# Optimization experiments

Hardware: AMD Instinct MI355X
Metric: run time of the kernel (lower is better)

## Reference

```python
import jax, jax.numpy as jnp
import numpy as np

B, T, P, H, LAT = 64, 256, 128, 512, 128


def _run_lstm(x, Wih, Whh, b, h0, c0):
    """Single unidirectional LSTM layer, PyTorch gate order (i,f,g,o).
    x: (B,T,in) -> outputs (B,T,H), final h (B,H)."""
    xW = jnp.einsum('bti,gi->btg', x, Wih) + b  # precompute input projection (B,T,4H)

    def step(carry, xw_t):
        h, c = carry
        g = xw_t + h @ Whh.T
        i, f, gg, o = jnp.split(g, 4, axis=-1)
        c = jax.nn.sigmoid(f) * c + jax.nn.sigmoid(i) * jnp.tanh(gg)
        h = jax.nn.sigmoid(o) * jnp.tanh(c)
        return (h, c), h

    (hT, cT), hs = jax.lax.scan(step, (h0, c0), jnp.swapaxes(xW, 0, 1))
    return jnp.swapaxes(hs, 0, 1), hT


def setup_inputs() -> dict:
    key = jax.random.key(0)
    ks = iter(jax.random.split(key, 40))
    rn = lambda shape, s=0.05: jax.random.normal(next(ks), shape, jnp.float32) * s
    inp = {
        'x': (jax.random.uniform(next(ks), (B, T, P)) < 0.1).astype(jnp.float32),
        'e0f_Wih': rn((4 * H, P)), 'e0f_Whh': rn((4 * H, H)), 'e0f_b': jnp.zeros((4 * H,), jnp.float32),
        'e0b_Wih': rn((4 * H, P)), 'e0b_Whh': rn((4 * H, H)), 'e0b_b': jnp.zeros((4 * H,), jnp.float32),
        'e1f_Wih': rn((4 * H, 2 * H)), 'e1f_Whh': rn((4 * H, H)), 'e1f_b': jnp.zeros((4 * H,), jnp.float32),
        'e1b_Wih': rn((4 * H, 2 * H)), 'e1b_Whh': rn((4 * H, H)), 'e1b_b': jnp.zeros((4 * H,), jnp.float32),
        'enc_fc_W': rn((LAT, 2 * H)), 'enc_fc_b': jnp.zeros((LAT,), jnp.float32),
        'dec_fc_W': rn((H, LAT)), 'dec_fc_b': jnp.zeros((H,), jnp.float32),
        'start_token': rn((1, 1, P), 0.1),
        'd0_Wih': rn((4 * H, P)), 'd0_Whh': rn((4 * H, H)), 'd0_b': jnp.zeros((4 * H,), jnp.float32),
        'd1_Wih': rn((4 * H, H)), 'd1_Whh': rn((4 * H, H)), 'd1_b': jnp.zeros((4 * H,), jnp.float32),
        'out_W': rn((P, H)), 'out_b': jnp.zeros((P,), jnp.float32),
        'teacher_forcing_ratio': 1,
    }
    return inp


def reference(x, e0f_Wih, e0f_Whh, e0f_b, e0b_Wih, e0b_Whh, e0b_b,
              e1f_Wih, e1f_Whh, e1f_b, e1b_Wih, e1b_Whh, e1b_b,
              enc_fc_W, enc_fc_b, dec_fc_W, dec_fc_b, start_token,
              d0_Wih, d0_Whh, d0_b, d1_Wih, d1_Whh, d1_b, out_W, out_b,
              teacher_forcing_ratio):
    b = x.shape[0]
    z0 = jnp.zeros((b, H), x.dtype)
    # ---- encoder: 2-layer bidirectional LSTM ----
    f0, _ = _run_lstm(x, e0f_Wih, e0f_Whh, e0f_b, z0, z0)
    r0, _ = _run_lstm(x[:, ::-1], e0b_Wih, e0b_Whh, e0b_b, z0, z0)
    l0 = jnp.concatenate([f0, r0[:, ::-1]], axis=-1)  # (B,T,2H)
    _, h_fwd = _run_lstm(l0, e1f_Wih, e1f_Whh, e1f_b, z0, z0)
    _, h_bwd = _run_lstm(l0[:, ::-1], e1b_Wih, e1b_Whh, e1b_b, z0, z0)
    z = jnp.concatenate([h_fwd, h_bwd], axis=-1) @ enc_fc_W.T + enc_fc_b  # (B,LAT)
    # ---- decoder: teacher-forced 2-layer LSTM ----
    h0d = z @ dec_fc_W.T + dec_fc_b  # (B,H), repeated for every layer
    xs = jnp.concatenate([jnp.broadcast_to(start_token, (b, 1, P)), x[:, :-1]], axis=1)
    o0, _ = _run_lstm(xs, d0_Wih, d0_Whh, d0_b, h0d, z0)
    o1, _ = _run_lstm(o0, d1_Wih, d1_Whh, d1_b, h0d, z0)
    x_hat = jax.nn.sigmoid(o1 @ out_W.T + out_b)  # (B,T,P)
    return x_hat, z
```

## Files before the change

kernel.cpp:

```cpp
#include <hip/hip_runtime.h>
#include <stdint.h>


typedef unsigned short u16;
typedef unsigned int u32;
typedef float f32x4 __attribute__((ext_vector_type(4)));
typedef __bf16 bf16x8 __attribute__((ext_vector_type(8)));
typedef unsigned int u32x4 __attribute__((ext_vector_type(4)));

#define AT_LD(p) __hip_atomic_load((p), __ATOMIC_RELAXED, __HIP_MEMORY_SCOPE_AGENT)
#define AT_ST(p, v) __hip_atomic_store((p), (v), __ATOMIC_RELAXED, __HIP_MEMORY_SCOPE_AGENT)

__device__ __forceinline__ u16 f2bf(float f) {
  u32 u = __builtin_bit_cast(u32, f);
  u += 0x7FFFu + ((u >> 16) & 1u);
  return (u16)(u >> 16);
}
__device__ __forceinline__ float bf2f(u16 h) {
  return __builtin_bit_cast(float, (u32)h << 16);
}
__device__ __forceinline__ bf16x8 ld8(const u16* p) {
  u32x4 v = *(const u32x4*)p;
  return __builtin_bit_cast(bf16x8, v);
}
__device__ __forceinline__ float sigf(float x) { return 1.f / (1.f + __expf(-x)); }
__device__ __forceinline__ float tanhx(float x) {
  x = fminf(fmaxf(x, -15.f), 15.f);
  float e = __expf(2.f * x);
  return (e - 1.f) / (e + 1.f);
}

__global__ void k_prep_x(const float* __restrict__ x, const float* __restrict__ st,
                         u16* __restrict__ Ax, u16* __restrict__ Axs, int n) {
  int i = blockIdx.x * 256 + threadIdx.x;
  if (i >= n) return;
  Ax[i] = f2bf(x[i]);
  int col = i & 127;
  int t = (i >> 7) & 255;
  float v = (t == 0) ? st[col] : x[i - 128];
  Axs[i] = f2bf(v);
}

struct CvtJobs {
  const float* src[13];
  u16* dst[13];
  int off[14];
};
__global__ void k_cvt_all(CvtJobs j, int total) {
  int i = blockIdx.x * 256 + threadIdx.x;
  if (i >= total) return;
  int a = 0;
#pragma unroll
  for (int k = 1; k < 13; ++k) a += (i >= j.off[k]) ? 1 : 0;
  int local = i - j.off[a];
  j.dst[a][local] = f2bf(j.src[a][local]);
}

__global__ __launch_bounds__(256) void k_gemm_bt(
    const u16* __restrict__ A, const u16* __restrict__ B, const float* __restrict__ bias,
    u16* __restrict__ Cb, float* __restrict__ Cf, int M, int N, int K, int sig) {
  __shared__ __align__(16) u16 As[128 * 64];
  __shared__ __align__(16) u16 Bs[128 * 64];
  const int m0 = blockIdx.x * 128, n0 = blockIdx.y * 128;
  const int tid = threadIdx.x, lane = tid & 63, wave = tid >> 6;
  const int wm = wave >> 1, wn = wave & 1;

  f32x4 acc[4][4];
#pragma unroll
  for (int i = 0; i < 4; ++i)
#pragma unroll
    for (int j = 0; j < 4; ++j) acc[i][j] = (f32x4){0.f, 0.f, 0.f, 0.f};

  const int nkt = K >> 6;
  for (int kt = 0; kt < nkt; ++kt) {
#pragma unroll
    for (int i = 0; i < 4; ++i) {
      int ch = tid + (i << 8);
      int row = ch >> 3, k8 = ch & 7;
      int dst = row * 128 + ((k8 * 16) ^ ((row & 7) << 4));
      u32x4 va = *(const u32x4*)(A + (size_t)(m0 + row) * K + kt * 64 + k8 * 8);
      *(u32x4*)((char*)As + dst) = va;
      u32x4 vb = *(const u32x4*)(B + (size_t)(n0 + row) * K + kt * 64 + k8 * 8);
      *(u32x4*)((char*)Bs + dst) = vb;
    }
    __syncthreads();
#pragma unroll
    for (int kk = 0; kk < 2; ++kk) {
      int kb = kk * 64 + ((lane >> 4) << 4);
      bf16x8 afr[4], bfr[4];
#pragma unroll
      for (int i = 0; i < 4; ++i) {
        int ra = wm * 64 + i * 16 + (lane & 15);
        afr[i] = ld8((const u16*)((const char*)As + ra * 128 + (kb ^ ((ra & 7) << 4))));
        int rb = wn * 64 + i * 16 + (lane & 15);
        bfr[i] = ld8((const u16*)((const char*)Bs + rb * 128 + (kb ^ ((rb & 7) << 4))));
      }
#pragma unroll
      for (int i = 0; i < 4; ++i)
#pragma unroll
        for (int j = 0; j < 4; ++j)
          acc[i][j] = __builtin_amdgcn_mfma_f32_16x16x32_bf16(afr[i], bfr[j], acc[i][j], 0, 0, 0);
    }
    __syncthreads();
  }
#pragma unroll
  for (int i = 0; i < 4; ++i) {
#pragma unroll
    for (int j = 0; j < 4; ++j) {
      int col = n0 + wn * 64 + j * 16 + (lane & 15);
      float bv = bias ? bias[col] : 0.f;
#pragma unroll
      for (int r = 0; r < 4; ++r) {
        int row = m0 + wm * 64 + i * 16 + ((lane >> 4) << 2) + r;
        float v = acc[i][j][r] + bv;
        if (sig) Cf[(size_t)row * N + col] = 1.f / (1.f + __expf(-v));
        else     Cb[(size_t)row * N + col] = f2bf(v);
      }
    }
  }
}

struct Rec2 {
  const u16* xW[8];
  const u16* Whh[8];
  const u16* Wih[8];
  const float* bias[8];
  const float* h0[8];
  u16* seq[8];
  float* hfin[8];
  u16* hxc[8];
  int prod[8];
  int seqstride[8]; int coloff[8]; int rev[8]; int hfinstride[8];
  int grp[8]; int fused[8]; int fullp[8];
  u32* tags;
};

__global__ __launch_bounds__(256, 1) void k_rec2(Rec2 p) {
  const int chain = blockIdx.x & 7;
  const int c = blockIdx.x >> 3;
  const int tid = threadIdx.x, lane = tid & 63, wave = tid >> 6;
  const int arow = lane & 15, kg = lane >> 4;

  const u16* __restrict__ xW = p.xW[chain];
  const u16* __restrict__ Whh = p.Whh[chain];
  const u16* __restrict__ Wih = p.Wih[chain];
  const float* __restrict__ bias = p.bias[chain];
  const float* __restrict__ h0 = p.h0[chain];
  u16* seq = p.seq[chain];
  float* hfin = p.hfin[chain];
  u32* hx = (u32*)p.hxc[chain];
  const u32* hxp = (const u32*)p.hxc[p.prod[chain]];
  const int grp = p.grp[chain], rev = p.rev[chain];
  const int fused = p.fused[chain], fullp = p.fullp[chain];
  const int sstride = p.seqstride[chain], coloff = p.coloff[chain];
  const int hstride = p.hfinstride[chain];
  u32* myt = p.tags + chain * 64;
  const u32* pt = p.tags + p.prod[chain] * 64;

  __shared__ __align__(16) u16 Wlds[64][64][8];
  __shared__ __align__(16) u16 Xlds[64][64][8];
  __shared__ __align__(16) u16 hbufA[8192];
  __shared__ float gbuf[4][16][16];
  __shared__ float cbuf[256];
  __shared__ float bbuf[64];

  for (int e = tid; e < 4096; e += 256) {
    int n = e >> 6, k8 = e & 63;
    int grow = ((n >> 4) << 9) + (c << 4) + (n & 15);
    *(u32x4*)(&Wlds[k8][n][0]) = *(const u32x4*)(Whh + (size_t)grow * 512 + k8 * 8);
    if (fused)
      *(u32x4*)(&Xlds[k8][n][0]) = *(const u32x4*)(Wih + (size_t)grow * 512 + k8 * 8);
  }
  if (tid < 64) bbuf[tid] = fused ? bias[((tid >> 4) << 9) + (c << 4) + (tid & 15)] : 0.f;
  cbuf[tid] = 0.f;
  if (tid < 128) {
    int row = tid >> 3, q = tid & 7;
    float a = 0.f, b2 = 0.f;
    if (h0) {
      a = h0[(size_t)(grp * 16 + row) * 512 + (c << 4) + 2 * q];
      b2 = h0[(size_t)(grp * 16 + row) * 512 + (c << 4) + 2 * q + 1];
    }
    u32 pk = (u32)f2bf(a) | ((u32)f2bf(b2) << 16);
    AT_ST(hx + (size_t)c * 128 + (row << 3) + q, pk);
  }
  asm volatile("s_waitcnt vmcnt(0)" ::: "memory");
  __syncthreads();
  if (tid == 0) AT_ST(myt + c, 1u);

  for (int t = 0; t < 256; ++t) {
    const int t_eff = rev ? 255 - t : t;
    const int slot = fullp ? t : (t & 3);
    const int slotn = fullp ? (t + 1) : ((t + 1) & 3);

    float xwv[4] = {0.f, 0.f, 0.f, 0.f};
    if (!fused) {
#pragma unroll
      for (int r4 = 0; r4 < 4; ++r4) {
        int row = (kg << 2) + r4;
        xwv[r4] = bf2f(xW[(((size_t)((grp * 16 + row) * 256 + t_eff)) << 11) +
                          (wave << 9) + (c << 4) + arow]);
      }
    }
    if (wave == 0) {
      u32 thr_own = (u32)(t + 1), thr_prod = (u32)(t + 2);
      while (true) {
        int ok = 1;
        if (lane < 32) {
          if (lane != c) ok = (AT_LD(myt + lane) >= thr_own);
        } else if (fused) {
          ok = (AT_LD(pt + (lane - 32)) >= thr_prod);
        }
        if (__all(ok)) break;
        __builtin_amdgcn_s_sleep(1);
      }
    }
    __syncthreads();
    __builtin_amdgcn_sched_barrier(0);

#pragma unroll
    for (int i = 0; i < 4; ++i) {
      int cid = tid + (i << 8);
      int row = cid >> 6, ch8 = cid & 63;
      const u32* src = hx + ((size_t)slot * 32 + (ch8 >> 1)) * 128 +
                       (row << 3) + ((ch8 & 1) << 2);
      u32x4 v;
      v.x = AT_LD(src + 0); v.y = AT_LD(src + 1);
      v.z = AT_LD(src + 2); v.w = AT_LD(src + 3);
      *(u32x4*)((char*)hbufA + row * 1024 + ((ch8 << 4) ^ ((row & 7) << 4))) = v;
    }
    bf16x8 xf[16];
    if (fused) {
#pragma unroll
      for (int kt = 0; kt < 16; ++kt) {
        const u32* hp = hxp + ((size_t)(t + 1) * 32 + 2 * kt + (kg >> 1)) * 128 +
                        (arow << 3) + ((kg & 1) << 2);
        u32x4 v;
        v.x = AT_LD(hp + 0); v.y = AT_LD(hp + 1);
        v.z = AT_LD(hp + 2); v.w = AT_LD(hp + 3);
        xf[kt] = __builtin_bit_cast(bf16x8, v);
      }
    }
    __syncthreads();

    bf16x8 af[16];
#pragma unroll
    for (int kt = 0; kt < 16; ++kt)
      af[kt] = ld8((const u16*)((const char*)hbufA + arow * 1024 +
                                ((kt * 64 + (kg << 4)) ^ ((arow & 7) << 4))));
    f32x4 ae = {0.f, 0.f, 0.f, 0.f}, ao = {0.f, 0.f, 0.f, 0.f};
#pragma unroll
    for (int kt = 0; kt < 16; ++kt) {
      bf16x8 bw = ld8(&Wlds[(kt << 2) + kg][(wave << 4) + arow][0]);
      if (kt & 1) ao = __builtin_amdgcn_mfma_f32_16x16x32_bf16(af[kt], bw, ao, 0, 0, 0);
      else        ae = __builtin_amdgcn_mfma_f32_16x16x32_bf16(af[kt], bw, ae, 0, 0, 0);
      if (fused) {
        bf16x8 bx = ld8(&Xlds[(kt << 2) + kg][(wave << 4) + arow][0]);
        if (kt & 1) ae = __builtin_amdgcn_mfma_f32_16x16x32_bf16(xf[kt], bx, ae, 0, 0, 0);
        else        ao = __builtin_amdgcn_mfma_f32_16x16x32_bf16(xf[kt], bx, ao, 0, 0, 0);
      }
    }
#pragma unroll
    for (int r4 = 0; r4 < 4; ++r4)
      gbuf[wave][(kg << 2) + r4][arow] = ae[r4] + ao[r4] + xwv[r4];
    __syncthreads();

    u32 pk = 0; int row2 = 0, j0 = 0;
    float hh0 = 0.f, hh1 = 0.f;
    if (tid >= 128) {
      int t2 = tid - 128;
      row2 = t2 >> 3; int q = t2 & 7; j0 = q << 1;
      float i0 = gbuf[0][row2][j0], i1 = gbuf[0][row2][j0 + 1];
      float f0 = gbuf[1][row2][j0], f1 = gbuf[1][row2][j0 + 1];
      float g0 = gbuf[2][row2][j0], g1 = gbuf[2][row2][j0 + 1];
      float o0v = gbuf[3][row2][j0], o1v = gbuf[3][row2][j0 + 1];
      if (fused) {
        i0 += bbuf[j0]; i1 += bbuf[j0 + 1];
        f0 += bbuf[16 + j0]; f1 += bbuf[16 + j0 + 1];
        g0 += bbuf[32 + j0]; g1 += bbuf[32 + j0 + 1];
        o0v += bbuf[48 + j0]; o1v += bbuf[48 + j0 + 1];
      }
      int ci = (row2 << 4) + j0;
      float cc0 = sigf(f0) * cbuf[ci] + sigf(i0) * tanhx(g0);
      float cc1 = sigf(f1) * cbuf[ci + 1] + sigf(i1) * tanhx(g1);
      cbuf[ci] = cc0; cbuf[ci + 1] = cc1;
      hh0 = sigf(o0v) * tanhx(cc0);
      hh1 = sigf(o1v) * tanhx(cc1);
      pk = (u32)f2bf(hh0) | ((u32)f2bf(hh1) << 16);
      AT_ST(hx + ((size_t)slotn * 32 + c) * 128 + (row2 << 3) + q, pk);
      asm volatile("s_waitcnt vmcnt(0)" ::: "memory");
    }
    __syncthreads();
    if (tid == 128) AT_ST(myt + c, (u32)(t + 2));
    if (tid >= 128) {
      if (seq)
        *(u32*)(seq + ((size_t)((grp * 16 + row2) * 256 + t_eff)) * sstride +
                coloff + (c << 4) + j0) = pk;
      if (hfin && t == 255) {
        hfin[(size_t)(grp * 16 + row2) * hstride + (c << 4) + j0] = hh0;
        hfin[(size_t)(grp * 16 + row2) * hstride + (c << 4) + j0 + 1] = hh1;
      }
    }
  }
}

__global__ void k_enc_head(const float* __restrict__ hcat, const float* __restrict__ W,
                           const float* __restrict__ b, float* __restrict__ zws,
                           float* __restrict__ zout) {
  int bi = blockIdx.x, j = threadIdx.x;
  const float* h = hcat + bi * 1024;
  const float* w = W + j * 1024;
  float s = b[j];
  for (int k = 0; k < 1024; ++k) s += h[k] * w[k];
  zws[bi * 128 + j] = s;
  zout[bi * 128 + j] = s;
}

__global__ void k_dec_head(const float* __restrict__ z, const float* __restrict__ W,
                           const float* __restrict__ b, float* __restrict__ h0d) {
  int bi = blockIdx.x, j = threadIdx.x;
  const float* zz = z + bi * 128;
  const float* w = W + j * 128;
  float s = b[j];
  for (int k = 0; k < 128; ++k) s += zz[k] * w[k];
  h0d[bi * 512 + j] = s;
}

extern "C" void kernel_launch(void* const* d_in, const int* in_sizes, int n_in,
                              void* d_out, int out_size, void* d_ws, size_t ws_size,
                              hipStream_t stream) {
  (void)in_sizes; (void)n_in; (void)out_size;
  const float* x        = (const float*)d_in[0];
  const float* e0f_Wih  = (const float*)d_in[1];
  const float* e0f_Whh  = (const float*)d_in[2];
  const float* e0f_b    = (const float*)d_in[3];
  const float* e0b_Wih  = (const float*)d_in[4];
  const float* e0b_Whh  = (const float*)d_in[5];
  const float* e0b_b    = (const float*)d_in[6];
  const float* e1f_Wih  = (const float*)d_in[7];
  const float* e1f_Whh  = (const float*)d_in[8];
  const float* e1f_b    = (const float*)d_in[9];
  const float* e1b_Wih  = (const float*)d_in[10];
  const float* e1b_Whh  = (const float*)d_in[11];
  const float* e1b_b    = (const float*)d_in[12];
  const float* enc_fc_W = (const float*)d_in[13];
  const float* enc_fc_b = (const float*)d_in[14];
  const float* dec_fc_W = (const float*)d_in[15];
  const float* dec_fc_b = (const float*)d_in[16];
  const float* start_tk = (const float*)d_in[17];
  const float* d0_Wih   = (const float*)d_in[18];
  const float* d0_Whh   = (const float*)d_in[19];
  const float* d0_b     = (const float*)d_in[20];
  const float* d1_Wih   = (const float*)d_in[21];
  const float* d1_Whh   = (const float*)d_in[22];
  const float* d1_b     = (const float*)d_in[23];
  const float* out_W    = (const float*)d_in[24];
  const float* out_b    = (const float*)d_in[25];

  uintptr_t base = (uintptr_t)d_ws;
  size_t off = 0;
  auto carve = [&](size_t bytes) -> void* {
    off = (off + 255) & ~(size_t)255;
    void* p = (void*)(base + off);
    off += bytes;
    return p;
  };
  u16* Ax     = (u16*)carve((size_t)2097152 * 2);
  u16* Axs    = (u16*)carve((size_t)2097152 * 2);
  u16* Wb_e0f = (u16*)carve((size_t)262144 * 2);
  u16* Wb_e0b = (u16*)carve((size_t)262144 * 2);
  u16* Wb_d0  = (u16*)carve((size_t)262144 * 2);
  u16* Wb_e1f = (u16*)carve((size_t)2097152 * 2);
  u16* Wb_e1b = (u16*)carve((size_t)2097152 * 2);
  u16* Wb_d1  = (u16*)carve((size_t)1048576 * 2);
  u16* Wb_out = (u16*)carve((size_t)65536 * 2);
  u16* Wh_e0f = (u16*)carve((size_t)1048576 * 2);
  u16* Wh_e0b = (u16*)carve((size_t)1048576 * 2);
  u16* Wh_e1f = (u16*)carve((size_t)1048576 * 2);
  u16* Wh_e1b = (u16*)carve((size_t)1048576 * 2);
  u16* Wh_d0  = (u16*)carve((size_t)1048576 * 2);
  u16* Wh_d1  = (u16*)carve((size_t)1048576 * 2);
  u16* slot0  = (u16*)carve((size_t)16384 * 2048 * 2);
  u16* slot1  = (u16*)carve((size_t)16384 * 2048 * 2);
  u16* l0     = (u16*)carve((size_t)33619968);
  u16* hxring = (u16*)carve((size_t)524288);
  float* hcat = (float*)carve((size_t)65536 * 4);
  float* zws  = (float*)carve((size_t)8192 * 4);
  float* h0d  = (float*)carve((size_t)32768 * 4);
  u32* tags0  = (u32*)carve(2048);
  u32* tags1  = (u32*)carve(2048);
  u32* tags2  = (u32*)carve(2048);
  if (off > ws_size) return;

  u16* o1     = l0;
  u16* hxprod = l0 + 8388608;

  (void)hipMemsetAsync(tags0, 0, 6144, stream);

  k_prep_x<<<8192, 256, 0, stream>>>(x, start_tk, Ax, Axs, 2097152);
  {
    CvtJobs j{};
    const float* s[13] = {e0f_Wih, e0b_Wih, d0_Wih, e1f_Wih, e1b_Wih, d1_Wih, out_W,
                          e0f_Whh, e0b_Whh, e1f_Whh, e1b_Whh, d0_Whh, d1_Whh};
    u16* d[13] = {Wb_e0f, Wb_e0b, Wb_d0, Wb_e1f, Wb_e1b, Wb_d1, Wb_out,
                  Wh_e0f, Wh_e0b, Wh_e1f, Wh_e1b, Wh_d0, Wh_d1};
    int n[13] = {262144, 262144, 262144, 2097152, 2097152, 1048576, 65536,
                 1048576, 1048576, 1048576, 1048576, 1048576, 1048576};
    int acc = 0;
    for (int k = 0; k < 13; ++k) { j.src[k] = s[k]; j.dst[k] = d[k]; j.off[k] = acc; acc += n[k]; }
    j.off[13] = acc;
    k_cvt_all<<<(acc + 255) / 256, 256, 0, stream>>>(j, acc);
  }

  k_gemm_bt<<<dim3(128, 16), 256, 0, stream>>>(Ax, Wb_e0f, e0f_b, slot0, nullptr, 16384, 2048, 128, 0);
  k_gemm_bt<<<dim3(128, 16), 256, 0, stream>>>(Ax, Wb_e0b, e0b_b, slot1, nullptr, 16384, 2048, 128, 0);
  {
    Rec2 r{};
    for (int ch = 0; ch < 8; ++ch) {
      int dir2 = ch >> 2, g = ch & 3;
      r.xW[ch] = dir2 ? slot1 : slot0;
      r.Whh[ch] = dir2 ? Wh_e0b : Wh_e0f;
      r.Wih[ch] = nullptr; r.bias[ch] = nullptr; r.h0[ch] = nullptr;
      r.seq[ch] = l0; r.seqstride[ch] = 1024; r.coloff[ch] = dir2 ? 512 : 0;
      r.rev[ch] = dir2; r.hfin[ch] = nullptr; r.hfinstride[ch] = 0;
      r.grp[ch] = g; r.fused[ch] = 0; r.fullp[ch] = 0; r.prod[ch] = 0;
      r.hxc[ch] = hxring + (size_t)ch * 32768;
    }
    r.tags = tags0;
    k_rec2<<<256, 256, 0, stream>>>(r);
  }
  k_gemm_bt<<<dim3(128, 16), 256, 0, stream>>>(l0, Wb_e1f, e1f_b, slot0, nullptr, 16384, 2048, 1024, 0);
  k_gemm_bt<<<dim3(128, 16), 256, 0, stream>>>(l0, Wb_e1b, e1b_b, slot1, nullptr, 16384, 2048, 1024, 0);
  {
    Rec2 r{};
    for (int ch = 0; ch < 8; ++ch) {
      int dir2 = ch >> 2, g = ch & 3;
      r.xW[ch] = dir2 ? slot1 : slot0;
      r.Whh[ch] = dir2 ? Wh_e1b : Wh_e1f;
      r.Wih[ch] = nullptr; r.bias[ch] = nullptr; r.h0[ch] = nullptr;
      r.seq[ch] = nullptr; r.seqstride[ch] = 0; r.coloff[ch] = 0;
      r.rev[ch] = dir2; r.hfin[ch] = hcat + (dir2 ? 512 : 0); r.hfinstride[ch] = 1024;
      r.grp[ch] = g; r.fused[ch] = 0; r.fullp[ch] = 0; r.prod[ch] = 0;
      r.hxc[ch] = hxring + (size_t)ch * 32768;
    }
    r.tags = tags1;
    k_rec2<<<256, 256, 0, stream>>>(r);
  }
  k_enc_head<<<64, 128, 0, stream>>>(hcat, enc_fc_W, enc_fc_b, zws, ((float*)d_out) + 2097152);
  k_dec_head<<<64, 512, 0, stream>>>(zws, dec_fc_W, dec_fc_b, h0d);
  k_gemm_bt<<<dim3(128, 16), 256, 0, stream>>>(Axs, Wb_d0, d0_b, slot0, nullptr, 16384, 2048, 128, 0);
  {
    Rec2 r{};
    for (int ch = 0; ch < 4; ++ch) {
      r.xW[ch] = slot0;
      r.Whh[ch] = Wh_d0;
      r.Wih[ch] = nullptr; r.bias[ch] = nullptr; r.h0[ch] = h0d;
      r.seq[ch] = nullptr; r.seqstride[ch] = 0; r.coloff[ch] = 0;
      r.rev[ch] = 0; r.hfin[ch] = nullptr; r.hfinstride[ch] = 0;
      r.grp[ch] = ch; r.fused[ch] = 0; r.fullp[ch] = 1; r.prod[ch] = 0;
      r.hxc[ch] = hxprod + (size_t)ch * 2105344;
    }
    for (int ch = 4; ch < 8; ++ch) {
      r.xW[ch] = nullptr;
      r.Whh[ch] = Wh_d1;
      r.Wih[ch] = Wb_d1; r.bias[ch] = d1_b; r.h0[ch] = h0d;
      r.seq[ch] = o1; r.seqstride[ch] = 512; r.coloff[ch] = 0;
      r.rev[ch] = 0; r.hfin[ch] = nullptr; r.hfinstride[ch] = 0;
      r.grp[ch] = ch - 4; r.fused[ch] = 1; r.fullp[ch] = 0; r.prod[ch] = ch - 4;
      r.hxc[ch] = hxring + (size_t)ch * 32768;
    }
    r.tags = tags2;
    k_rec2<<<256, 256, 0, stream>>>(r);
  }
  k_gemm_bt<<<dim3(128, 1), 256, 0, stream>>>(o1, Wb_out, out_b, nullptr, (float*)d_out, 16384, 128, 512, 1);
}
```

Measured before the change: 5.477 ms.

## Add dedicated encoder recurrence kernel with 16 blocks per chain

Adds a specialized encoder LSTM recurrence kernel that uses 128 blocks instead of 256. Each chain now spans 16 blocks, and each block owns 32 hidden columns across all four gates. The block holds its Whh slice in LDS, runs the gate GEMM with MFMA, applies the cell update and publishes h through a global ring buffer with tag-based inter-block sync. The aim is to cut the number of blocks each timestep must synchronise with and to drop the generic fused/prod branches. The cost is more recurrent work per block and a heavy LDS footprint from the 128 KB weight slice.

```diff
diff --git a/kernel.cpp b/kernel.cpp
--- a/kernel.cpp
+++ b/kernel.cpp
@@ -115,6 +115,149 @@
         float v = acc[i][j][r] + bv;
         if (sig) Cf[(size_t)row * N + col] = 1.f / (1.f + __expf(-v));
         else     Cb[(size_t)row * N + col] = f2bf(v);
+      }
+    }
+  }
+}
+
+struct RecE {
+  const u16* xW[8];
+  const u16* Whh[8];
+  u16* seq[8];
+  float* hfin[8];
+  u16* hxc[8];
+  int seqstride[8]; int coloff[8]; int rev[8]; int hfinstride[8];
+  int grp[8];
+  u32* tags;
+};
+
+__global__ __launch_bounds__(256, 1) void k_rec_e(RecE p) {
+  const int chain = blockIdx.x & 7;
+  const int c = blockIdx.x >> 3;
+  const int tid = threadIdx.x, lane = tid & 63, wave = tid >> 6;
+  const int arow = lane & 15, kg = lane >> 4;
+
+  const u16* __restrict__ xW = p.xW[chain];
+  const u16* __restrict__ Whh = p.Whh[chain];
+  u16* seq = p.seq[chain];
+  float* hfin = p.hfin[chain];
+  u32* hx = (u32*)p.hxc[chain];
+  const int grp = p.grp[chain], rev = p.rev[chain];
+  const int sstride = p.seqstride[chain], coloff = p.coloff[chain];
+  const int hstride = p.hfinstride[chain];
+  u32* myt = p.tags + chain * 64;
+
+  __shared__ __align__(16) u16 Wlds[64][128][8];
+  __shared__ __align__(16) u16 hbufA[8192];
+  __shared__ float gbuf[4][16][32];
+  __shared__ float cbuf[512];
+
+  for (int e = tid; e < 8192; e += 256) {
+    int n = e >> 6, k8 = e & 63;
+    int grow = ((n >> 5) << 9) + (c << 5) + (n & 31);
+    *(u32x4*)(&Wlds[k8][n][0]) = *(const u32x4*)(Whh + (size_t)grow * 512 + k8 * 8);
+  }
+  for (int e = tid; e < 512; e += 256) cbuf[e] = 0.f;
+  for (int e = tid; e < 4096; e += 256) AT_ST(hx + e, 0u);
+  asm volatile("s_waitcnt vmcnt(0)" ::: "memory");
+  __syncthreads();
+  if (tid == 0) AT_ST(myt + c, 1u);
+
+  for (int t = 0; t < 256; ++t) {
+    const int t_eff = rev ? 255 - t : t;
+    const int slot = t & 3;
+    const int slotn = (t + 1) & 3;
+
+    float xwv[4][2];
+#pragma unroll
+    for (int r4 = 0; r4 < 4; ++r4) {
+      int row = (kg << 2) + r4;
+      const u16* xwp = xW + (((size_t)((grp * 16 + row) * 256 + t_eff)) << 11) +
+                       (wave << 9) + (c << 5);
+      xwv[r4][0] = bf2f(xwp[arow]);
+      xwv[r4][1] = bf2f(xwp[arow + 16]);
+    }
+    if (wave == 0) {
+      u32 thr = (u32)(t + 1);
+      while (true) {
+        int ok = 1;
+        if (lane < 16 && lane != c) ok = (AT_LD(myt + lane) >= thr);
+        if (__all(ok)) break;
+        __builtin_amdgcn_s_sleep(1);
+      }
+    }
+    __syncthreads();
+    __builtin_amdgcn_sched_barrier(0);
+
+#pragma unroll
+    for (int i = 0; i < 4; ++i) {
+      int cid = tid + (i << 8);
+      int row = cid >> 6, ch8 = cid & 63;
+      const u32* src = hx + slot * 4096 + row * 256 + ch8 * 4;
+      u32x4 v;
+      v.x = AT_LD(src + 0); v.y = AT_LD(src + 1);
+      v.z = AT_LD(src + 2); v.w = AT_LD(src + 3);
+      *(u32x4*)((char*)hbufA + row * 1024 + ((ch8 << 4) ^ ((row & 7) << 4))) = v;
+    }
+    __syncthreads();
+
+    bf16x8 af[16];
+#pragma unroll
+    for (int kt = 0; kt < 16; ++kt)
+      af[kt] = ld8((const u16*)((const char*)hbufA + arow * 1024 +
+                                ((kt * 64 + (kg << 4)) ^ ((arow & 7) << 4))));
+    f32x4 acc0 = {0.f, 0.f, 0.f, 0.f};
+    f32x4 acc1 = {0.f, 0.f, 0.f, 0.f};
+#pragma unroll
+    for (int kt = 0; kt < 16; ++kt) {
+      const u16* bp = &Wlds[(kt << 2) + kg][(wave << 5) + arow][0];
+      bf16x8 b0 = ld8(bp);
+      bf16x8 b1 = ld8(bp + 128);
+      acc0 = __builtin_amdgcn_mfma_f32_16x16x32_bf16(af[kt], b0, acc0, 0, 0, 0);
+      acc1 = __builtin_amdgcn_mfma_f32_16x16x32_bf16(af[kt], b1, acc1, 0, 0, 0);
+    }
+#pragma unroll
+    for (int r4 = 0; r4 < 4; ++r4) {
+      gbuf[wave][(kg << 2) + r4][arow] = acc0[r4] + xwv[r4][0];
+      gbuf[wave][(kg << 2) + r4][arow + 16] = acc1[r4] + xwv[r4][1];
+    }
+    __syncthreads();
+
+    u32 pk0 = 0, pk1 = 0; int row2 = 0, j0 = 0;
+    float hhv[4] = {0.f, 0.f, 0.f, 0.f};
+    if (tid >= 128) {
+      int t2 = tid - 128;
+      row2 = t2 >> 3; int q = t2 & 7; j0 = q << 2;
+#pragma unroll
+      for (int jj = 0; jj < 4; ++jj) {
+        int col = j0 + jj;
+        float iv = gbuf[0][row2][col];
+        float fv = gbuf[1][row2][col];
+        float gv = gbuf[2][row2][col];
+        float ov = gbuf[3][row2][col];
+        int ci = (row2 << 5) + col;
+        float cc = sigf(fv) * cbuf[ci] + sigf(iv) * tanhx(gv);
+        cbuf[ci] = cc;
+        hhv[jj] = sigf(ov) * tanhx(cc);
+      }
+      pk0 = (u32)f2bf(hhv[0]) | ((u32)f2bf(hhv[1]) << 16);
+      pk1 = (u32)f2bf(hhv[2]) | ((u32)f2bf(hhv[3]) << 16);
+      u32* dst = hx + slotn * 4096 + row2 * 256 + (c << 4) + (q << 1);
+      AT_ST(dst, pk0);
+      AT_ST(dst + 1, pk1);
+      asm volatile("s_waitcnt vmcnt(0)" ::: "memory");
+    }
+    __syncthreads();
+    if (tid == 128) AT_ST(myt + c, (u32)(t + 2));
+    if (tid >= 128) {
+      if (seq) {
+        u32* sp = (u32*)(seq + ((size_t)((grp * 16 + row2) * 256 + t_eff)) * sstride +
+                         coloff + (c << 5) + j0);
+        sp[0] = pk0; sp[1] = pk1;
+      }
+      if (hfin && t == 255) {
+        float* hp = hfin + (size_t)(grp * 16 + row2) * hstride + (c << 5) + j0;
+        hp[0] = hhv[0]; hp[1] = hhv[1]; hp[2] = hhv[2]; hp[3] = hhv[3];
       }
     }
   }
@@ -414,36 +557,34 @@
   k_gemm_bt<<<dim3(128, 16), 256, 0, stream>>>(Ax, Wb_e0f, e0f_b, slot0, nullptr, 16384, 2048, 128, 0);
   k_gemm_bt<<<dim3(128, 16), 256, 0, stream>>>(Ax, Wb_e0b, e0b_b, slot1, nullptr, 16384, 2048, 128, 0);
   {
-    Rec2 r{};
+    RecE r{};
     for (int ch = 0; ch < 8; ++ch) {
       int dir2 = ch >> 2, g = ch & 3;
       r.xW[ch] = dir2 ? slot1 : slot0;
       r.Whh[ch] = dir2 ? Wh_e0b : Wh_e0f;
-      r.Wih[ch] = nullptr; r.bias[ch] = nullptr; r.h0[ch] = nullptr;
       r.seq[ch] = l0; r.seqstride[ch] = 1024; r.coloff[ch] = dir2 ? 512 : 0;
       r.rev[ch] = dir2; r.hfin[ch] = nullptr; r.hfinstride[ch] = 0;
-      r.grp[ch] = g; r.fused[ch] = 0; r.fullp[ch] = 0; r.prod[ch] = 0;
+      r.grp[ch] = g;
       r.hxc[ch] = hxring + (size_t)ch * 32768;
     }
     r.tags = tags0;
-    k_rec2<<<256, 256, 0, stream>>>(r);
+    k_rec_e<<<128, 256, 0, stream>>>(r);
   }
   k_gemm_bt<<<dim3(128, 16), 256, 0, stream>>>(l0, Wb_e1f, e1f_b, slot0, nullptr, 16384, 2048, 1024, 0);
   k_gemm_bt<<<dim3(128, 16), 256, 0, stream>>>(l0, Wb_e1b, e1b_b, slot1, nullptr, 16384, 2048, 1024, 0);
   {
-    Rec2 r{};
+    RecE r{};
     for (int ch = 0; ch < 8; ++ch) {
       int dir2 = ch >> 2, g = ch & 3;
       r.xW[ch] = dir2 ? slot1 : slot0;
       r.Whh[ch] = dir2 ? Wh_e1b : Wh_e1f;
-      r.Wih[ch] = nullptr; r.bias[ch] = nullptr; r.h0[ch] = nullptr;
       r.seq[ch] = nullptr; r.seqstride[ch] = 0; r.coloff[ch] = 0;
       r.rev[ch] = dir2; r.hfin[ch] = hcat + (dir2 ? 512 : 0); r.hfinstride[ch] = 1024;
-      r.grp[ch] = g; r.fused[ch] = 0; r.fullp[ch] = 0; r.prod[ch] = 0;
+      r.grp[ch] = g;
       r.hxc[ch] = hxring + (size_t)ch * 32768;
     }
     r.tags = tags1;
-    k_rec2<<<256, 256, 0, stream>>>(r);
+    k_rec_e<<<128, 256, 0, stream>>>(r);
   }
   k_enc_head<<<64, 128, 0, stream>>>(hcat, enc_fc_W, enc_fc_b, zws, ((float*)d_out) + 2097152);
   k_dec_head<<<64, 512, 0, stream>>>(zws, dec_fc_W, dec_fc_b, h0d);
```

After: 5.147 ms, median of 2. -6.0%, faster.
